# Performance work log

Hardware: AMD Instinct MI355X
Metric: run time of the kernel (lower is better)

The kernel has to match this reference:

```python
import jax, jax.numpy as jnp
import numpy as np

DIM = 512
INNER = 512  # heads*dim_head = 8*64
SCALE = 64 ** -0.5  # dim_head^{-0.5}, applied to BOTH q and k as in the source


def setup_inputs() -> dict:
    key = jax.random.key(0)
    k1, k2, k3, k4 = jax.random.split(key, 4)
    x = jax.random.normal(k1, (8, 2048, DIM), dtype=jnp.float32)
    Wqkv = jax.random.normal(k2, (DIM, 3 * INNER), dtype=jnp.float32) * (DIM ** -0.5)
    Wout = jax.random.normal(k3, (INNER, DIM), dtype=jnp.float32) * (INNER ** -0.5)
    bout = jax.random.normal(k4, (DIM,), dtype=jnp.float32) * 0.01
    return {"x": x, "Wqkv": Wqkv, "Wout": Wout, "bout": bout}


def reference(x, Wqkv, Wout, bout):
    # fused QKV projection (no bias)
    qkv = jnp.einsum("bnd,de->bne", x, Wqkv)
    q, k, v = jnp.split(qkv, 3, axis=-1)
    # note: source scales BOTH q and k by dim_head^{-0.5}
    scores = jnp.einsum("bnd,bmd->bnm", q * SCALE, k * SCALE)  # [B,N,N]
    attn = jax.nn.softmax(scores, axis=-1)
    out = jnp.einsum("bnm,bmd->bnd", attn, v)
    # residual add, then output projection (dropout=0.0 -> identity)
    return jnp.einsum("bnd,de->bne", out + x, Wout) + bout
```

## Files before the change

kernel.cpp:

```cpp
#include <hip/hip_runtime.h>
#include <hip/hip_bf16.h>


typedef __attribute__((ext_vector_type(8))) short bf16x8;
typedef __attribute__((ext_vector_type(4))) float f32x4;

__device__ __forceinline__ unsigned short f2bf(float f) {
  unsigned u = __builtin_bit_cast(unsigned, f);
  u += 0x7fffu + ((u >> 16) & 1u);
  return (unsigned short)(u >> 16);
}
__device__ __forceinline__ float bf2f(unsigned short h) {
  unsigned u = ((unsigned)h) << 16;
  return __builtin_bit_cast(float, u);
}

__device__ __forceinline__ void async16(const unsigned short* g, unsigned short* l) {
  __builtin_amdgcn_global_load_lds(
      (const __attribute__((address_space(1))) unsigned int*)g,
      (__attribute__((address_space(3))) unsigned int*)l, 16, 0, 0);
}

__global__ __launch_bounds__(256) void prep_x(const float* __restrict__ X,
                                              unsigned short* __restrict__ XB) {
  const size_t base = ((size_t)blockIdx.x * 256 + threadIdx.x) * 16;
  f32x4 a0 = *(const f32x4*)&X[base];
  f32x4 a1 = *(const f32x4*)&X[base + 4];
  f32x4 a2 = *(const f32x4*)&X[base + 8];
  f32x4 a3 = *(const f32x4*)&X[base + 12];
  bf16x8 o0, o1;
#pragma unroll
  for (int j = 0; j < 4; ++j) {
    o0[j] = (short)f2bf(a0[j]);
    o0[4 + j] = (short)f2bf(a1[j]);
    o1[j] = (short)f2bf(a2[j]);
    o1[4 + j] = (short)f2bf(a3[j]);
  }
  *(bf16x8*)&XB[base] = o0;
  *(bf16x8*)&XB[base + 8] = o1;
}

__global__ __launch_bounds__(256) void prep_w(const float* __restrict__ W,
                                              unsigned short* __restrict__ WT) {
  const int t = threadIdx.x;
  const int c0 = blockIdx.x * 128 + (t & 15) * 8;
  const int k0 = blockIdx.y * 128 + (t >> 4) * 8;
  float r[8][8];
#pragma unroll
  for (int j = 0; j < 8; ++j) {
    f32x4 lo = *(const f32x4*)&W[(size_t)(k0 + j) * 1536 + c0];
    f32x4 hi = *(const f32x4*)&W[(size_t)(k0 + j) * 1536 + c0 + 4];
#pragma unroll
    for (int q = 0; q < 4; ++q) {
      r[j][q] = lo[q];
      r[j][4 + q] = hi[q];
    }
  }
#pragma unroll
  for (int i = 0; i < 8; ++i) {
    const float scl = (c0 + i < 1024) ? 0.125f : 1.0f;
    bf16x8 o;
#pragma unroll
    for (int j = 0; j < 8; ++j) o[j] = (short)f2bf(r[j][i] * scl);
    *(bf16x8*)&WT[(size_t)(c0 + i) * 512 + k0] = o;
  }
}

__global__ __launch_bounds__(256) void transpose_wout(const float* __restrict__ W,
                                                      unsigned short* __restrict__ WT) {
  const int t = threadIdx.x;
  const int c0 = blockIdx.x * 128 + (t & 15) * 8;
  const int k0 = blockIdx.y * 128 + (t >> 4) * 8;
  float r[8][8];
#pragma unroll
  for (int j = 0; j < 8; ++j) {
    f32x4 lo = *(const f32x4*)&W[(size_t)(k0 + j) * 512 + c0];
    f32x4 hi = *(const f32x4*)&W[(size_t)(k0 + j) * 512 + c0 + 4];
#pragma unroll
    for (int q = 0; q < 4; ++q) {
      r[j][q] = lo[q];
      r[j][4 + q] = hi[q];
    }
  }
#pragma unroll
  for (int i = 0; i < 8; ++i) {
    bf16x8 o;
#pragma unroll
    for (int j = 0; j < 8; ++j) o[j] = (short)f2bf(r[j][i]);
    *(bf16x8*)&WT[(size_t)(c0 + i) * 512 + k0] = o;
  }
}

__global__ __launch_bounds__(256) void transpose_v(const unsigned short* __restrict__ QKV,
                                                   unsigned short* __restrict__ VT) {
  const int t = threadIdx.x;
  const int m0 = blockIdx.x * 128 + (t & 15) * 8;
  const int d0 = blockIdx.y * 128 + (t >> 4) * 8;
  bf16x8 r[8];
#pragma unroll
  for (int j = 0; j < 8; ++j)
    r[j] = *(const bf16x8*)&QKV[(size_t)(m0 + j) * 1536 + 1024 + d0];
#pragma unroll
  for (int i = 0; i < 8; ++i) {
    bf16x8 o;
#pragma unroll
    for (int j = 0; j < 8; ++j) o[j] = r[j][i];
    *(bf16x8*)&VT[(size_t)(d0 + i) * 16384 + m0] = o;
  }
}


#define GEMM97_BODY(AG, ASTR, BG, BSTR, KDIM)                                            \
  __shared__ __align__(16) unsigned short Asm[4096];                                     \
  __shared__ __align__(16) unsigned short Bsm[4096];                                     \
  const int tid = threadIdx.x;                                                           \
  const int wave = tid >> 6, lane = tid & 63;                                            \
  const int wr = wave >> 1, wc = wave & 1;                                               \
  const int lg = lane >> 4, ll = lane & 15;                                              \
  const int kk = lg * 8;                                                                 \
  const int srow = wave * 32 + (lane >> 2);          \
  const int scol = (lane & 3) * 8;                           \
  f32x4 acc[4][4];                                                                       \
  _Pragma("unroll") for (int i = 0; i < 4; ++i) _Pragma("unroll") for (int j = 0; j < 4; \
                                                                       ++j) acc[i][j] =  \
      (f32x4){0.f, 0.f, 0.f, 0.f};                                                       \
  for (int kt = 0; kt < KDIM; kt += 32) {                                                \
    async16(&AG[(size_t)srow * ASTR + kt + scol], &Asm[wave * 1024]);                    \
    async16(&AG[(size_t)(srow + 16) * ASTR + kt + scol], &Asm[wave * 1024 + 512]);       \
    async16(&BG[(size_t)srow * BSTR + kt + scol], &Bsm[wave * 1024]);                    \
    async16(&BG[(size_t)(srow + 16) * BSTR + kt + scol], &Bsm[wave * 1024 + 512]);       \
    __syncthreads();                            \
    bf16x8 af[4], bfr[4];                                                                \
    _Pragma("unroll") for (int ai = 0; ai < 4; ++ai) af[ai] =                            \
        *(const bf16x8*)&Asm[(wr * 64 + ai * 16 + ll) * 32 + kk];                        \
    _Pragma("unroll") for (int bj = 0; bj < 4; ++bj) bfr[bj] =                           \
        *(const bf16x8*)&Bsm[(wc * 64 + bj * 16 + ll) * 32 + kk];                        \
    _Pragma("unroll") for (int ai = 0; ai < 4; ++ai) _Pragma("unroll") for (int bj = 0;  \
                                                                            bj < 4;      \
                                                                            ++bj)        \
        acc[ai][bj] =                                                                    \
        __builtin_amdgcn_mfma_f32_16x16x32_bf16(af[ai], bfr[bj], acc[ai][bj], 0, 0, 0);  \
    __syncthreads();                    \
  }

__global__ __launch_bounds__(256) void gemm_qkv97(const unsigned short* __restrict__ XB,
                                                  const unsigned short* __restrict__ WT,
                                                  unsigned short* __restrict__ QKV) {
  const int bid = blockIdx.x;
  const int qt = bid / 12, nt = bid - qt * 12;
  const unsigned short* Ag = XB + (size_t)(qt * 128) * 512;
  const unsigned short* Bg = WT + (size_t)(nt * 128) * 512;
  GEMM97_BODY(Ag, 512, Bg, 512, 512)
#pragma unroll
  for (int ai = 0; ai < 4; ++ai)
#pragma unroll
    for (int bj = 0; bj < 4; ++bj) {
      const int col = nt * 128 + wc * 64 + bj * 16 + ll;
#pragma unroll
      for (int r = 0; r < 4; ++r) {
        const int row = qt * 128 + wr * 64 + ai * 16 + lg * 4 + r;
        QKV[(size_t)row * 1536 + col] = f2bf(acc[ai][bj][r]);
      }
    }
}

__global__ __launch_bounds__(256) void sgemm97(const unsigned short* __restrict__ QKV,
                                               unsigned short* __restrict__ S) {
  const int bid = blockIdx.x;
  const int b = bid & 7;
  const int idx = bid >> 3;
  const int kvt = idx & 15, qt = idx >> 4;
  const unsigned short* Ag = QKV + ((size_t)b * 2048 + qt * 128) * 1536;
  const unsigned short* Bg = QKV + ((size_t)b * 2048 + kvt * 128) * 1536 + 512;
  GEMM97_BODY(Ag, 1536, Bg, 1536, 512)
  unsigned short* Sg = S + (size_t)b * 2048 * 2048;
#pragma unroll
  for (int ai = 0; ai < 4; ++ai)
#pragma unroll
    for (int bj = 0; bj < 4; ++bj) {
      const int col = kvt * 128 + wc * 64 + bj * 16 + ll;
#pragma unroll
      for (int r = 0; r < 4; ++r) {
        const int row = qt * 128 + wr * 64 + ai * 16 + lg * 4 + r;
        Sg[(size_t)row * 2048 + col] = f2bf(acc[ai][bj][r]);
      }
    }
}

__global__ __launch_bounds__(256) void pvgemm97(const unsigned short* __restrict__ P,
                                                const unsigned short* __restrict__ VT,
                                                const float* __restrict__ X,
                                                unsigned short* __restrict__ RES) {
  const int bid = blockIdx.x;
  const int b = bid & 7;
  const int idx = bid >> 3;
  const int dt = idx & 3, qt = idx >> 2;
  const unsigned short* Ag = P + (size_t)b * 2048 * 2048 + (size_t)(qt * 128) * 2048;
  const unsigned short* Bg = VT + (size_t)(dt * 128) * 16384 + (size_t)b * 2048;
  GEMM97_BODY(Ag, 2048, Bg, 16384, 2048)
#pragma unroll
  for (int ai = 0; ai < 4; ++ai)
#pragma unroll
    for (int bj = 0; bj < 4; ++bj) {
      const int col = dt * 128 + wc * 64 + bj * 16 + ll;
#pragma unroll
      for (int r = 0; r < 4; ++r) {
        const size_t row = (size_t)b * 2048 + qt * 128 + wr * 64 + ai * 16 + lg * 4 + r;
        const float val = acc[ai][bj][r] + X[row * 512 + col];
        RES[row * 1536 + 1024 + col] = f2bf(val);
      }
    }
}

__global__ __launch_bounds__(256) void gemm_out97(const unsigned short* __restrict__ A,
                                                  const unsigned short* __restrict__ WT,
                                                  const float* __restrict__ bias,
                                                  float* __restrict__ OUT) {
  const int bid = blockIdx.x;
  const int dt = bid & 3, qt = bid >> 2;
  const unsigned short* Ag = A + (size_t)(qt * 128) * 1536 + 1024;
  const unsigned short* Bg = WT + (size_t)(dt * 128) * 512;
  GEMM97_BODY(Ag, 1536, Bg, 512, 512)
#pragma unroll
  for (int ai = 0; ai < 4; ++ai)
#pragma unroll
    for (int bj = 0; bj < 4; ++bj) {
      const int col = dt * 128 + wc * 64 + bj * 16 + ll;
      const float bv = bias[col];
#pragma unroll
      for (int r = 0; r < 4; ++r) {
        const int row = qt * 128 + wr * 64 + ai * 16 + lg * 4 + r;
        OUT[(size_t)row * 512 + col] = acc[ai][bj][r] + bv;
      }
    }
}

__global__ __launch_bounds__(256) void softmax_rows(unsigned short* __restrict__ S) {
  __shared__ float red[8];
  const int tid = threadIdx.x;
  const int wave = tid >> 6, lane = tid & 63;
  unsigned short* row = S + (size_t)blockIdx.x * 2048;

  bf16x8 v = *(const bf16x8*)&row[tid * 8];
  float f[8];
#pragma unroll
  for (int j = 0; j < 8; ++j) f[j] = bf2f((unsigned short)v[j]);

  float mx = f[0];
#pragma unroll
  for (int j = 1; j < 8; ++j) mx = fmaxf(mx, f[j]);
  mx = fmaxf(mx, __shfl_xor(mx, 1));
  mx = fmaxf(mx, __shfl_xor(mx, 2));
  mx = fmaxf(mx, __shfl_xor(mx, 4));
  mx = fmaxf(mx, __shfl_xor(mx, 8));
  mx = fmaxf(mx, __shfl_xor(mx, 16));
  mx = fmaxf(mx, __shfl_xor(mx, 32));
  if (lane == 0) red[wave] = mx;
  __syncthreads();
  mx = fmaxf(fmaxf(red[0], red[1]), fmaxf(red[2], red[3]));

  float s = 0.f;
#pragma unroll
  for (int j = 0; j < 8; ++j) {
    f[j] = __expf(f[j] - mx);
    s += f[j];
  }
  s += __shfl_xor(s, 1);
  s += __shfl_xor(s, 2);
  s += __shfl_xor(s, 4);
  s += __shfl_xor(s, 8);
  s += __shfl_xor(s, 16);
  s += __shfl_xor(s, 32);
  if (lane == 0) red[4 + wave] = s;
  __syncthreads();
  s = (red[4] + red[5]) + (red[6] + red[7]);
  const float inv = 1.0f / s;
#pragma unroll
  for (int j = 0; j < 8; ++j) v[j] = (short)f2bf(f[j] * inv);
  *(bf16x8*)&row[tid * 8] = v;
}

extern "C" void kernel_launch(void* const* d_in, const int* in_sizes, int n_in,
                              void* d_out, int out_size, void* d_ws, size_t ws_size,
                              hipStream_t stream) {
  const float* x = (const float*)d_in[0];
  const float* Wqkv = (const float*)d_in[1];
  const float* Wout = (const float*)d_in[2];
  const float* bout = (const float*)d_in[3];
  float* out = (float*)d_out;

  unsigned short* qkvb = (unsigned short*)d_ws;
  unsigned short* VT = qkvb + (size_t)16384 * 1536;
  unsigned short* S = VT + (size_t)512 * 16384;
  unsigned short* xb = S;
  unsigned short* WT = S + (size_t)16384 * 512;
  unsigned short* WoutT = VT;

  prep_x<<<2048, 256, 0, stream>>>(x, xb);
  prep_w<<<dim3(12, 4), 256, 0, stream>>>(Wqkv, WT);
  gemm_qkv97<<<1536, 256, 0, stream>>>(xb, WT, qkvb);
  transpose_v<<<dim3(128, 4), 256, 0, stream>>>(qkvb, VT);
  sgemm97<<<2048, 256, 0, stream>>>(qkvb, S);
  softmax_rows<<<16384, 256, 0, stream>>>(S);
  pvgemm97<<<512, 256, 0, stream>>>(S, VT, x, qkvb);
  transpose_wout<<<dim3(4, 4), 256, 0, stream>>>(Wout, WoutT);
  gemm_out97<<<512, 256, 0, stream>>>(qkvb, WoutT, bout, out);
}
```

Before: 201.0 us.

## Fuse softmax into score and PV GEMMs with double-buffered LDS pipelines

The standalone softmax pass over the 8x2048x2048 score matrix is removed. The score GEMM now emits per-tile row max and sum partials, a small combine kernel reduces them to a per-row max and inverse sum, and the PV GEMM applies the exponent and normalisation while staging the A tile into LDS. The GEMMs also gain double-buffered async LDS loads and launch_bounds occupancy hints, so the next tile's loads overlap compute. The cost is extra exp work inside the PV loop and a scratch buffer placed in the output region.

New measurement: 221.3 us. 1.1x slower.

```diff
diff --git a/kernel.cpp b/kernel.cpp
--- a/kernel.cpp
+++ b/kernel.cpp
@@ -110,47 +110,59 @@
 }
 
 
-#define GEMM97_BODY(AG, ASTR, BG, BSTR, KDIM)                                            \
-  __shared__ __align__(16) unsigned short Asm[4096];                                     \
-  __shared__ __align__(16) unsigned short Bsm[4096];                                     \
-  const int tid = threadIdx.x;                                                           \
-  const int wave = tid >> 6, lane = tid & 63;                                            \
-  const int wr = wave >> 1, wc = wave & 1;                                               \
-  const int lg = lane >> 4, ll = lane & 15;                                              \
-  const int kk = lg * 8;                                                                 \
-  const int srow = wave * 32 + (lane >> 2);          \
-  const int scol = (lane & 3) * 8;                           \
+#define GEMM97_VARS                                            \
+  const int tid = threadIdx.x;                                 \
+  const int wave = tid >> 6, lane = tid & 63;                  \
+  const int wr = wave >> 1, wc = wave & 1;                     \
+  const int lg = lane >> 4, ll = lane & 15;                    \
+  const int kk = lg * 8;                                       \
+  const int srow = wave * 32 + (lane >> 2);                    \
+  const int scol = (lane & 3) * 8;
+
+#define GEMM97DB_BODY(AG, ASTR, BG, BSTR, KDIM)                                          \
+  __shared__ __align__(16) unsigned short Asm[2][4096];                                  \
+  __shared__ __align__(16) unsigned short Bsm[2][4096];                                  \
+  GEMM97_VARS                                                                            \
   f32x4 acc[4][4];                                                                       \
   _Pragma("unroll") for (int i = 0; i < 4; ++i) _Pragma("unroll") for (int j = 0; j < 4; \
                                                                        ++j) acc[i][j] =  \
       (f32x4){0.f, 0.f, 0.f, 0.f};                                                       \
+  async16(&AG[(size_t)srow * ASTR + scol], &Asm[0][wave * 1024]);                        \
+  async16(&AG[(size_t)(srow + 16) * ASTR + scol], &Asm[0][wave * 1024 + 512]);           \
+  async16(&BG[(size_t)srow * BSTR + scol], &Bsm[0][wave * 1024]);                        \
+  async16(&BG[(size_t)(srow + 16) * BSTR + scol], &Bsm[0][wave * 1024 + 512]);           \
+  int cur = 0;                                                                           \
   for (int kt = 0; kt < KDIM; kt += 32) {                                                \
-    async16(&AG[(size_t)srow * ASTR + kt + scol], &Asm[wave * 1024]);                    \
-    async16(&AG[(size_t)(srow + 16) * ASTR + kt + scol], &Asm[wave * 1024 + 512]);       \
-    async16(&BG[(size_t)srow * BSTR + kt + scol], &Bsm[wave * 1024]);                    \
-    async16(&BG[(size_t)(srow + 16) * BSTR + kt + scol], &Bsm[wave * 1024 + 512]);       \
-    __syncthreads();                            \
+    __syncthreads();                                                                     \
+    if (kt + 32 < KDIM) {                                                                \
+      async16(&AG[(size_t)srow * ASTR + kt + 32 + scol], &Asm[cur ^ 1][wave * 1024]);    \
+      async16(&AG[(size_t)(srow + 16) * ASTR + kt + 32 + scol],                          \
+              &Asm[cur ^ 1][wave * 1024 + 512]);                                         \
+      async16(&BG[(size_t)srow * BSTR + kt + 32 + scol], &Bsm[cur ^ 1][wave * 1024]);    \
+      async16(&BG[(size_t)(srow + 16) * BSTR + kt + 32 + scol],                          \
+              &Bsm[cur ^ 1][wave * 1024 + 512]);                                         \
+    }                                                                                    \
     bf16x8 af[4], bfr[4];                                                                \
     _Pragma("unroll") for (int ai = 0; ai < 4; ++ai) af[ai] =                            \
-        *(const bf16x8*)&Asm[(wr * 64 + ai * 16 + ll) * 32 + kk];                        \
+        *(const bf16x8*)&Asm[cur][(wr * 64 + ai * 16 + ll) * 32 + kk];                   \
     _Pragma("unroll") for (int bj = 0; bj < 4; ++bj) bfr[bj] =                           \
-        *(const bf16x8*)&Bsm[(wc * 64 + bj * 16 + ll) * 32 + kk];                        \
+        *(const bf16x8*)&Bsm[cur][(wc * 64 + bj * 16 + ll) * 32 + kk];                   \
     _Pragma("unroll") for (int ai = 0; ai < 4; ++ai) _Pragma("unroll") for (int bj = 0;  \
                                                                             bj < 4;      \
                                                                             ++bj)        \
         acc[ai][bj] =                                                                    \
         __builtin_amdgcn_mfma_f32_16x16x32_bf16(af[ai], bfr[bj], acc[ai][bj], 0, 0, 0);  \
-    __syncthreads();                    \
-  }
-
-__global__ __launch_bounds__(256) void gemm_qkv97(const unsigned short* __restrict__ XB,
-                                                  const unsigned short* __restrict__ WT,
-                                                  unsigned short* __restrict__ QKV) {
+    cur ^= 1;                                                                            \
+  }
+
+__global__ __launch_bounds__(256, 3) void gemm_qkv97(const unsigned short* __restrict__ XB,
+                                                     const unsigned short* __restrict__ WT,
+                                                     unsigned short* __restrict__ QKV) {
   const int bid = blockIdx.x;
   const int qt = bid / 12, nt = bid - qt * 12;
   const unsigned short* Ag = XB + (size_t)(qt * 128) * 512;
   const unsigned short* Bg = WT + (size_t)(nt * 128) * 512;
-  GEMM97_BODY(Ag, 512, Bg, 512, 512)
+  GEMM97DB_BODY(Ag, 512, Bg, 512, 512)
 #pragma unroll
   for (int ai = 0; ai < 4; ++ai)
 #pragma unroll
@@ -164,15 +176,52 @@
     }
 }
 
-__global__ __launch_bounds__(256) void sgemm97(const unsigned short* __restrict__ QKV,
-                                               unsigned short* __restrict__ S) {
+__global__ __launch_bounds__(256, 3) void sgemm97(const unsigned short* __restrict__ QKV,
+                                                  unsigned short* __restrict__ S,
+                                                  float* __restrict__ part) {
   const int bid = blockIdx.x;
   const int b = bid & 7;
   const int idx = bid >> 3;
   const int kvt = idx & 15, qt = idx >> 4;
   const unsigned short* Ag = QKV + ((size_t)b * 2048 + qt * 128) * 1536;
   const unsigned short* Bg = QKV + ((size_t)b * 2048 + kvt * 128) * 1536 + 512;
-  GEMM97_BODY(Ag, 1536, Bg, 1536, 512)
+  GEMM97DB_BODY(Ag, 1536, Bg, 1536, 512)
+
+  __syncthreads();
+  float* sc = (float*)&Asm[0][0];
+#pragma unroll
+  for (int ai = 0; ai < 4; ++ai)
+#pragma unroll
+    for (int r = 0; r < 4; ++r) {
+      float mx = fmaxf(fmaxf(acc[ai][0][r], acc[ai][1][r]), fmaxf(acc[ai][2][r], acc[ai][3][r]));
+      mx = fmaxf(mx, __shfl_xor(mx, 1));
+      mx = fmaxf(mx, __shfl_xor(mx, 2));
+      mx = fmaxf(mx, __shfl_xor(mx, 4));
+      mx = fmaxf(mx, __shfl_xor(mx, 8));
+      float se = __expf(acc[ai][0][r] - mx) + __expf(acc[ai][1][r] - mx) +
+                 __expf(acc[ai][2][r] - mx) + __expf(acc[ai][3][r] - mx);
+      se += __shfl_xor(se, 1);
+      se += __shfl_xor(se, 2);
+      se += __shfl_xor(se, 4);
+      se += __shfl_xor(se, 8);
+      if (ll == 0) {
+        const int rl = wave * 64 + ai * 16 + lg * 4 + r;
+        sc[rl * 2] = mx;
+        sc[rl * 2 + 1] = se;
+      }
+    }
+  __syncthreads();
+  if (tid < 128) {
+    const int wrr = tid >> 6, rl = tid & 63;
+    const float m0 = sc[((wrr * 2 + 0) * 64 + rl) * 2], l0 = sc[((wrr * 2 + 0) * 64 + rl) * 2 + 1];
+    const float m1 = sc[((wrr * 2 + 1) * 64 + rl) * 2], l1 = sc[((wrr * 2 + 1) * 64 + rl) * 2 + 1];
+    const float m = fmaxf(m0, m1);
+    const float l = l0 * __expf(m0 - m) + l1 * __expf(m1 - m);
+    const int rowg = b * 2048 + qt * 128 + tid;
+    part[(size_t)rowg * 32 + kvt * 2] = m;
+    part[(size_t)rowg * 32 + kvt * 2 + 1] = l;
+  }
+
   unsigned short* Sg = S + (size_t)b * 2048 * 2048;
 #pragma unroll
   for (int ai = 0; ai < 4; ++ai)
@@ -187,17 +236,85 @@
     }
 }
 
-__global__ __launch_bounds__(256) void pvgemm97(const unsigned short* __restrict__ P,
-                                                const unsigned short* __restrict__ VT,
-                                                const float* __restrict__ X,
-                                                unsigned short* __restrict__ RES) {
+__global__ __launch_bounds__(256) void combine_ml(const float* __restrict__ part,
+                                                  float* __restrict__ ml) {
+  const int row = blockIdx.x * 256 + threadIdx.x;
+  float mt[16], lt[16];
+#pragma unroll
+  for (int t = 0; t < 16; ++t) {
+    mt[t] = part[(size_t)row * 32 + t * 2];
+    lt[t] = part[(size_t)row * 32 + t * 2 + 1];
+  }
+  float m = mt[0];
+#pragma unroll
+  for (int t = 1; t < 16; ++t) m = fmaxf(m, mt[t]);
+  float l = 0.f;
+#pragma unroll
+  for (int t = 0; t < 16; ++t) l += lt[t] * __expf(mt[t] - m);
+  ml[row * 2] = m;
+  ml[row * 2 + 1] = 1.0f / l;
+}
+
+__global__ __launch_bounds__(256, 3) void pvgemm97(const unsigned short* __restrict__ S,
+                                                   const unsigned short* __restrict__ VT,
+                                                   const float* __restrict__ X,
+                                                   const float* __restrict__ ml,
+                                                   unsigned short* __restrict__ RES) {
+  __shared__ __align__(16) unsigned short Asm[4096];
+  __shared__ __align__(16) unsigned short Bsm[2][4096];
   const int bid = blockIdx.x;
   const int b = bid & 7;
   const int idx = bid >> 3;
   const int dt = idx & 3, qt = idx >> 2;
-  const unsigned short* Ag = P + (size_t)b * 2048 * 2048 + (size_t)(qt * 128) * 2048;
+  const unsigned short* Ag = S + (size_t)b * 2048 * 2048 + (size_t)(qt * 128) * 2048;
   const unsigned short* Bg = VT + (size_t)(dt * 128) * 16384 + (size_t)b * 2048;
-  GEMM97_BODY(Ag, 2048, Bg, 16384, 2048)
+  GEMM97_VARS
+  f32x4 acc[4][4];
+#pragma unroll
+  for (int i = 0; i < 4; ++i)
+#pragma unroll
+    for (int j = 0; j < 4; ++j) acc[i][j] = (f32x4){0.f, 0.f, 0.f, 0.f};
+
+  const int rowg0 = b * 2048 + qt * 128 + srow;
+  const float m0 = ml[rowg0 * 2], il0 = ml[rowg0 * 2 + 1];
+  const float m1 = ml[(rowg0 + 16) * 2], il1 = ml[(rowg0 + 16) * 2 + 1];
+
+  bf16x8 a0 = *(const bf16x8*)&Ag[(size_t)srow * 2048 + scol];
+  bf16x8 a1 = *(const bf16x8*)&Ag[(size_t)(srow + 16) * 2048 + scol];
+  async16(&Bg[(size_t)srow * 16384 + scol], &Bsm[0][wave * 1024]);
+  async16(&Bg[(size_t)(srow + 16) * 16384 + scol], &Bsm[0][wave * 1024 + 512]);
+  int cur = 0;
+
+  for (int kt = 0; kt < 2048; kt += 32) {
+    __syncthreads();
+    bf16x8 p0, p1;
+#pragma unroll
+    for (int j = 0; j < 8; ++j) {
+      p0[j] = (short)f2bf(__expf(bf2f((unsigned short)a0[j]) - m0) * il0);
+      p1[j] = (short)f2bf(__expf(bf2f((unsigned short)a1[j]) - m1) * il1);
+    }
+    *(bf16x8*)&Asm[srow * 32 + scol] = p0;
+    *(bf16x8*)&Asm[(srow + 16) * 32 + scol] = p1;
+    __syncthreads();
+    if (kt + 32 < 2048) {
+      async16(&Bg[(size_t)srow * 16384 + kt + 32 + scol], &Bsm[cur ^ 1][wave * 1024]);
+      async16(&Bg[(size_t)(srow + 16) * 16384 + kt + 32 + scol], &Bsm[cur ^ 1][wave * 1024 + 512]);
+      a0 = *(const bf16x8*)&Ag[(size_t)srow * 2048 + kt + 32 + scol];
+      a1 = *(const bf16x8*)&Ag[(size_t)(srow + 16) * 2048 + kt + 32 + scol];
+    }
+    bf16x8 af[4], bfr[4];
+#pragma unroll
+    for (int ai = 0; ai < 4; ++ai) af[ai] = *(const bf16x8*)&Asm[(wr * 64 + ai * 16 + ll) * 32 + kk];
+#pragma unroll
+    for (int bj = 0; bj < 4; ++bj)
+      bfr[bj] = *(const bf16x8*)&Bsm[cur][(wc * 64 + bj * 16 + ll) * 32 + kk];
+#pragma unroll
+    for (int ai = 0; ai < 4; ++ai)
+#pragma unroll
+      for (int bj = 0; bj < 4; ++bj)
+        acc[ai][bj] = __builtin_amdgcn_mfma_f32_16x16x32_bf16(af[ai], bfr[bj], acc[ai][bj], 0, 0, 0);
+    cur ^= 1;
+  }
 #pragma unroll
   for (int ai = 0; ai < 4; ++ai)
 #pragma unroll
@@ -212,15 +329,15 @@
     }
 }
 
-__global__ __launch_bounds__(256) void gemm_out97(const unsigned short* __restrict__ A,
-                                                  const unsigned short* __restrict__ WT,
-                                                  const float* __restrict__ bias,
-                                                  float* __restrict__ OUT) {
+__global__ __launch_bounds__(256, 3) void gemm_out97(const unsigned short* __restrict__ A,
+                                                     const unsigned short* __restrict__ WT,
+                                                     const float* __restrict__ bias,
+                                                     float* __restrict__ OUT) {
   const int bid = blockIdx.x;
   const int dt = bid & 3, qt = bid >> 2;
   const unsigned short* Ag = A + (size_t)(qt * 128) * 1536 + 1024;
   const unsigned short* Bg = WT + (size_t)(dt * 128) * 512;
-  GEMM97_BODY(Ag, 1536, Bg, 512, 512)
+  GEMM97DB_BODY(Ag, 1536, Bg, 512, 512)
 #pragma unroll
   for (int ai = 0; ai < 4; ++ai)
 #pragma unroll
@@ -233,51 +350,6 @@
         OUT[(size_t)row * 512 + col] = acc[ai][bj][r] + bv;
       }
     }
-}
-
-__global__ __launch_bounds__(256) void softmax_rows(unsigned short* __restrict__ S) {
-  __shared__ float red[8];
-  const int tid = threadIdx.x;
-  const int wave = tid >> 6, lane = tid & 63;
-  unsigned short* row = S + (size_t)blockIdx.x * 2048;
-
-  bf16x8 v = *(const bf16x8*)&row[tid * 8];
-  float f[8];
-#pragma unroll
-  for (int j = 0; j < 8; ++j) f[j] = bf2f((unsigned short)v[j]);
-
-  float mx = f[0];
-#pragma unroll
-  for (int j = 1; j < 8; ++j) mx = fmaxf(mx, f[j]);
-  mx = fmaxf(mx, __shfl_xor(mx, 1));
-  mx = fmaxf(mx, __shfl_xor(mx, 2));
-  mx = fmaxf(mx, __shfl_xor(mx, 4));
-  mx = fmaxf(mx, __shfl_xor(mx, 8));
-  mx = fmaxf(mx, __shfl_xor(mx, 16));
-  mx = fmaxf(mx, __shfl_xor(mx, 32));
-  if (lane == 0) red[wave] = mx;
-  __syncthreads();
-  mx = fmaxf(fmaxf(red[0], red[1]), fmaxf(red[2], red[3]));
-
-  float s = 0.f;
-#pragma unroll
-  for (int j = 0; j < 8; ++j) {
-    f[j] = __expf(f[j] - mx);
-    s += f[j];
-  }
-  s += __shfl_xor(s, 1);
-  s += __shfl_xor(s, 2);
-  s += __shfl_xor(s, 4);
-  s += __shfl_xor(s, 8);
-  s += __shfl_xor(s, 16);
-  s += __shfl_xor(s, 32);
-  if (lane == 0) red[4 + wave] = s;
-  __syncthreads();
-  s = (red[4] + red[5]) + (red[6] + red[7]);
-  const float inv = 1.0f / s;
-#pragma unroll
-  for (int j = 0; j < 8; ++j) v[j] = (short)f2bf(f[j] * inv);
-  *(bf16x8*)&row[tid * 8] = v;
 }
 
 extern "C" void kernel_launch(void* const* d_in, const int* in_sizes, int n_in,
@@ -295,14 +367,16 @@
   unsigned short* xb = S;
   unsigned short* WT = S + (size_t)16384 * 512;
   unsigned short* WoutT = VT;
+  float* part = out;
+  float* ml = out + (size_t)16384 * 32;
 
   prep_x<<<2048, 256, 0, stream>>>(x, xb);
   prep_w<<<dim3(12, 4), 256, 0, stream>>>(Wqkv, WT);
   gemm_qkv97<<<1536, 256, 0, stream>>>(xb, WT, qkvb);
   transpose_v<<<dim3(128, 4), 256, 0, stream>>>(qkvb, VT);
-  sgemm97<<<2048, 256, 0, stream>>>(qkvb, S);
-  softmax_rows<<<16384, 256, 0, stream>>>(S);
-  pvgemm97<<<512, 256, 0, stream>>>(S, VT, x, qkvb);
+  sgemm97<<<2048, 256, 0, stream>>>(qkvb, S, part);
+  combine_ml<<<64, 256, 0, stream>>>(part, ml);
+  pvgemm97<<<512, 256, 0, stream>>>(S, VT, x, ml, qkvb);
   transpose_wout<<<dim3(4, 4), 256, 0, stream>>>(Wout, WoutT);
   gemm_out97<<<512, 256, 0, stream>>>(qkvb, WoutT, bout, out);
 }
```
